# Kernel tuning notes

Hardware: AMD Instinct MI355X
Metric: run time of the kernel (lower is better)

Reference implementation:

```python
import jax, jax.numpy as jnp
import numpy as np

N, C, H, W = 64, 64, 128, 128
KH, KW = 3, 3


def setup_inputs() -> dict:
    key = jax.random.key(0)
    k1, k2 = jax.random.split(key)
    images = jax.random.normal(k1, (N, C, H, W), dtype=jnp.float32)
    kernels = jax.random.normal(k2, (N, C, KH, KW), dtype=jnp.float32)
    return {"images": images, "kernels": kernels}


def reference(images, kernels):
    # Per-sample conv: image i ([C,H,W]) convolved with kernel i ([C,kh,kw]) -> 1 channel.
    # Equivalent to a grouped conv with N groups:
    #   input  [1, N*C, H, W], weights [N, C, kh, kw], feature_group_count=N
    n, c, h, w = images.shape
    x = images.reshape(1, n * c, h, w)
    out = jax.lax.conv_general_dilated(
        x, kernels,
        window_strides=(1, 1),
        padding='VALID',
        dimension_numbers=('NCHW', 'OIHW', 'NCHW'),
        feature_group_count=n,
    )  # [1, N, H', W']
    return out.reshape(n, 1, out.shape[2], out.shape[3])
```

## Files before the change

### kernel.cpp

```cpp
#include <hip/hip_runtime.h>


#define NS   64
#define CCH  64
#define HH   128
#define WW   128
#define OHH  126
#define OWW  126
#define CHS  (HH * WW)

__global__ __launch_bounds__(256, 2)
void ImageWiseConv2d_direct(const float* __restrict__ img,
                            const float* __restrict__ ker,
                            float* __restrict__ out)
{
    const int tid = threadIdx.x;
    const int bx  = blockIdx.x;
    const int bt  = bx & 7;
    const int n   = bx >> 3;
    const int h0  = bt * 16;

    const int r0 = (tid >> 5) << 1;
    const int c0 = (tid & 31) << 2;

    int ihr = h0 + r0;
    if (ihr > HH - 4) ihr = HH - 4;

    const float* p0 = img + (((n * CCH) * HH) + ihr) * WW + c0;
    const float* kp = ker + (n * CCH) * 9;

    float a00 = 0.f, a01 = 0.f, a02 = 0.f, a03 = 0.f;
    float a10 = 0.f, a11 = 0.f, a12 = 0.f, a13 = 0.f;

    float4 A0, A1, A2, A3;
    A0 = *(const float4*)(p0);
    A1 = *(const float4*)(p0 + WW);
    A2 = *(const float4*)(p0 + 2 * WW);
    A3 = *(const float4*)(p0 + 3 * WW);

    for (int c = 0; c < CCH; ++c) {
        float4 nA0, nA1, nA2, nA3;
        const bool more = (c + 1 < CCH);
        if (more) {
            const float* q = p0 + (c + 1) * CHS;
            nA0 = *(const float4*)(q);
            nA1 = *(const float4*)(q + WW);
            nA2 = *(const float4*)(q + 2 * WW);
            nA3 = *(const float4*)(q + 3 * WW);
        }

        const float w0 = kp[c * 9 + 0], w1 = kp[c * 9 + 1], w2 = kp[c * 9 + 2];
        const float w3 = kp[c * 9 + 3], w4 = kp[c * 9 + 4], w5 = kp[c * 9 + 5];
        const float w6 = kp[c * 9 + 6], w7 = kp[c * 9 + 7], w8 = kp[c * 9 + 8];

        const float h40 = __shfl_down(A0.x, 1), h50 = __shfl_down(A0.y, 1);
        const float h41 = __shfl_down(A1.x, 1), h51 = __shfl_down(A1.y, 1);
        const float h42 = __shfl_down(A2.x, 1), h52 = __shfl_down(A2.y, 1);
        const float h43 = __shfl_down(A3.x, 1), h53 = __shfl_down(A3.y, 1);

        {
            const float v0 = A0.x, v1 = A0.y, v2 = A0.z, v3 = A0.w, v4 = h40, v5 = h50;
            a00 = fmaf(w0, v0, a00); a00 = fmaf(w1, v1, a00); a00 = fmaf(w2, v2, a00);
            a01 = fmaf(w0, v1, a01); a01 = fmaf(w1, v2, a01); a01 = fmaf(w2, v3, a01);
            a02 = fmaf(w0, v2, a02); a02 = fmaf(w1, v3, a02); a02 = fmaf(w2, v4, a02);
            a03 = fmaf(w0, v3, a03); a03 = fmaf(w1, v4, a03); a03 = fmaf(w2, v5, a03);
        }
        {
            const float v0 = A1.x, v1 = A1.y, v2 = A1.z, v3 = A1.w, v4 = h41, v5 = h51;
            a00 = fmaf(w3, v0, a00); a00 = fmaf(w4, v1, a00); a00 = fmaf(w5, v2, a00);
            a01 = fmaf(w3, v1, a01); a01 = fmaf(w4, v2, a01); a01 = fmaf(w5, v3, a01);
            a02 = fmaf(w3, v2, a02); a02 = fmaf(w4, v3, a02); a02 = fmaf(w5, v4, a02);
            a03 = fmaf(w3, v3, a03); a03 = fmaf(w4, v4, a03); a03 = fmaf(w5, v5, a03);
            a10 = fmaf(w0, v0, a10); a10 = fmaf(w1, v1, a10); a10 = fmaf(w2, v2, a10);
            a11 = fmaf(w0, v1, a11); a11 = fmaf(w1, v2, a11); a11 = fmaf(w2, v3, a11);
            a12 = fmaf(w0, v2, a12); a12 = fmaf(w1, v3, a12); a12 = fmaf(w2, v4, a12);
            a13 = fmaf(w0, v3, a13); a13 = fmaf(w1, v4, a13); a13 = fmaf(w2, v5, a13);
        }
        {
            const float v0 = A2.x, v1 = A2.y, v2 = A2.z, v3 = A2.w, v4 = h42, v5 = h52;
            a00 = fmaf(w6, v0, a00); a00 = fmaf(w7, v1, a00); a00 = fmaf(w8, v2, a00);
            a01 = fmaf(w6, v1, a01); a01 = fmaf(w7, v2, a01); a01 = fmaf(w8, v3, a01);
            a02 = fmaf(w6, v2, a02); a02 = fmaf(w7, v3, a02); a02 = fmaf(w8, v4, a02);
            a03 = fmaf(w6, v3, a03); a03 = fmaf(w7, v4, a03); a03 = fmaf(w8, v5, a03);
            a10 = fmaf(w3, v0, a10); a10 = fmaf(w4, v1, a10); a10 = fmaf(w5, v2, a10);
            a11 = fmaf(w3, v1, a11); a11 = fmaf(w4, v2, a11); a11 = fmaf(w5, v3, a11);
            a12 = fmaf(w3, v2, a12); a12 = fmaf(w4, v3, a12); a12 = fmaf(w5, v4, a12);
            a13 = fmaf(w3, v3, a13); a13 = fmaf(w4, v4, a13); a13 = fmaf(w5, v5, a13);
        }
        {
            const float v0 = A3.x, v1 = A3.y, v2 = A3.z, v3 = A3.w, v4 = h43, v5 = h53;
            a10 = fmaf(w6, v0, a10); a10 = fmaf(w7, v1, a10); a10 = fmaf(w8, v2, a10);
            a11 = fmaf(w6, v1, a11); a11 = fmaf(w7, v2, a11); a11 = fmaf(w8, v3, a11);
            a12 = fmaf(w6, v2, a12); a12 = fmaf(w7, v3, a12); a12 = fmaf(w8, v4, a12);
            a13 = fmaf(w6, v3, a13); a13 = fmaf(w7, v4, a13); a13 = fmaf(w8, v5, a13);
        }

        if (more) {
            A0 = nA0; A1 = nA1; A2 = nA2; A3 = nA3;
        }
    }

    const int oh0 = h0 + r0;
    if (oh0 < OHH) {
        float* o0 = out + (n * OHH + oh0) * OWW + c0;
        float* o1 = o0 + OWW;
        *(float2*)o0 = make_float2(a00, a01);
        *(float2*)o1 = make_float2(a10, a11);
        if (c0 < 124) {
            *(float2*)(o0 + 2) = make_float2(a02, a03);
            *(float2*)(o1 + 2) = make_float2(a12, a13);
        }
    }
}

extern "C" void kernel_launch(void* const* d_in, const int* in_sizes, int n_in,
                              void* d_out, int out_size, void* d_ws, size_t ws_size,
                              hipStream_t stream) {
    const float* img = (const float*)d_in[0];
    const float* ker = (const float*)d_in[1];
    float* out = (float*)d_out;

    ImageWiseConv2d_direct<<<dim3(NS * 8), dim3(256), 0, stream>>>(img, ker, out);
}
```

Baseline: 354.9 us.

## Stage input channel tiles into double-buffered LDS via async global_load_lds

Replaces per-thread overlapping register loads of four input rows with a cooperative, double-buffered LDS staging of an 18-row channel slab using direct global-to-LDS loads. Each thread then reads its four rows from shared memory. The aim is to remove redundant global loads, since the old scheme reads every row twice because neighbouring thread rows overlap, and to overlap the next channel's fetch with compute. In exchange it adds two barriers per channel and hand-written vmcnt waits whose counts must match the number of outstanding loads per thread; lanes that issue a different number of loads make this fragile.

Result: no change. 360.5 us (+1.6%).

```diff
diff --git a/kernel.cpp b/kernel.cpp
--- a/kernel.cpp
+++ b/kernel.cpp
@@ -1,53 +1,86 @@
 #include <hip/hip_runtime.h>
 
 
-#define NS   64
-#define CCH  64
-#define HH   128
-#define WW   128
-#define OHH  126
-#define OWW  126
-#define CHS  (HH * WW)
+#define NS    64
+#define CCH   64
+#define HH    128
+#define WW    128
+#define OHH   126
+#define OWW   126
+#define CHS   (HH * WW)
+#define WROWS 18
+#define WFLT  (WROWS * WW)
+
+#define STAGE_CH(dbuf, cc)                                                          \
+    {                                                                               \
+        const float* chb_ = imgn + (cc) * CHS;                                      \
+        {                                  \
+            const int e_ = wid * 64 + lane;                                         \
+            const float* s_ = chb_ + (h0 + (e_ >> 5)) * WW + (e_ & 31) * 4;         \
+            __builtin_amdgcn_global_load_lds(                                       \
+                (const __attribute__((address_space(1))) void*)s_,                  \
+                (__attribute__((address_space(3))) void*)&(dbuf)[(wid * 64) * 4],   \
+                16, 0, 0);                                                          \
+        }                                                                           \
+        {                               \
+            const int e_ = 256 + wid * 64 + lane;                                   \
+            const float* s_ = chb_ + (h0 + (e_ >> 5)) * WW + (e_ & 31) * 4;         \
+            __builtin_amdgcn_global_load_lds(                                       \
+                (const __attribute__((address_space(1))) void*)s_,                  \
+                (__attribute__((address_space(3))) void*)&(dbuf)[(256 + wid * 64) * 4], \
+                16, 0, 0);                                                          \
+        }                                                                           \
+        if (lane < 16) {  \
+            const int e_ = 512 + wid * 16 + lane;                                   \
+            int srow_ = h0 + (e_ >> 5);                                             \
+            if (srow_ > HH - 1) srow_ = HH - 1;                                     \
+            const float* s_ = chb_ + srow_ * WW + (e_ & 31) * 4;                    \
+            __builtin_amdgcn_global_load_lds(                                       \
+                (const __attribute__((address_space(1))) void*)s_,                  \
+                (__attribute__((address_space(3))) void*)&(dbuf)[(512 + wid * 16) * 4], \
+                16, 0, 0);                                                          \
+        }                                                                           \
+    }
 
 __global__ __launch_bounds__(256, 2)
-void ImageWiseConv2d_direct(const float* __restrict__ img,
-                            const float* __restrict__ ker,
-                            float* __restrict__ out)
+void ImageWiseConv2d_lds(const float* __restrict__ img,
+                         const float* __restrict__ ker,
+                         float* __restrict__ out)
 {
-    const int tid = threadIdx.x;
-    const int bx  = blockIdx.x;
-    const int bt  = bx & 7;
-    const int n   = bx >> 3;
-    const int h0  = bt * 16;
+    __shared__ float buf[2][WFLT];
+
+    const int tid  = threadIdx.x;
+    const int lane = tid & 63;
+    const int wid  = tid >> 6;
+    const int bx   = blockIdx.x;
+    const int bt   = bx & 7;
+    const int n    = bx >> 3;
+    const int h0   = bt * 16;
 
     const int r0 = (tid >> 5) << 1;
     const int c0 = (tid & 31) << 2;
 
-    int ihr = h0 + r0;
-    if (ihr > HH - 4) ihr = HH - 4;
-
-    const float* p0 = img + (((n * CCH) * HH) + ihr) * WW + c0;
-    const float* kp = ker + (n * CCH) * 9;
+    const float* imgn = img + (size_t)(n * CCH) * CHS;
+    const float* kp   = ker + n * CCH * 9;
 
     float a00 = 0.f, a01 = 0.f, a02 = 0.f, a03 = 0.f;
     float a10 = 0.f, a11 = 0.f, a12 = 0.f, a13 = 0.f;
 
-    float4 A0, A1, A2, A3;
-    A0 = *(const float4*)(p0);
-    A1 = *(const float4*)(p0 + WW);
-    A2 = *(const float4*)(p0 + 2 * WW);
-    A3 = *(const float4*)(p0 + 3 * WW);
+    STAGE_CH(buf[0], 0);
 
     for (int c = 0; c < CCH; ++c) {
-        float4 nA0, nA1, nA2, nA3;
-        const bool more = (c + 1 < CCH);
-        if (more) {
-            const float* q = p0 + (c + 1) * CHS;
-            nA0 = *(const float4*)(q);
-            nA1 = *(const float4*)(q + WW);
-            nA2 = *(const float4*)(q + 2 * WW);
-            nA3 = *(const float4*)(q + 3 * WW);
+        if (c + 1 < CCH) {
+            STAGE_CH(buf[(c + 1) & 1], c + 1);
+            asm volatile("s_waitcnt vmcnt(3)\n\ts_barrier" ::: "memory");
+        } else {
+            asm volatile("s_waitcnt vmcnt(0)\n\ts_barrier" ::: "memory");
         }
+
+        const float* cb = &buf[c & 1][r0 * WW + c0];
+        const float4 A0 = *(const float4*)(cb);
+        const float4 A1 = *(const float4*)(cb + WW);
+        const float4 A2 = *(const float4*)(cb + 2 * WW);
+        const float4 A3 = *(const float4*)(cb + 3 * WW);
 
         const float w0 = kp[c * 9 + 0], w1 = kp[c * 9 + 1], w2 = kp[c * 9 + 2];
         const float w3 = kp[c * 9 + 3], w4 = kp[c * 9 + 4], w5 = kp[c * 9 + 5];
@@ -95,9 +128,7 @@
             a13 = fmaf(w6, v3, a13); a13 = fmaf(w7, v4, a13); a13 = fmaf(w8, v5, a13);
         }
 
-        if (more) {
-            A0 = nA0; A1 = nA1; A2 = nA2; A3 = nA3;
-        }
+        asm volatile("s_barrier" ::: "memory");
     }
 
     const int oh0 = h0 + r0;
@@ -120,5 +151,5 @@
     const float* ker = (const float*)d_in[1];
     float* out = (float*)d_out;
 
-    ImageWiseConv2d_direct<<<dim3(NS * 8), dim3(256), 0, stream>>>(img, ker, out);
+    ImageWiseConv2d_lds<<<dim3(NS * 8), dim3(256), 0, stream>>>(img, ker, out);
 }
```
